# Optimization experiments

Measured on AMD Instinct MI355X. Metric: run time of the kernel, lower is better.

The kernel has to match this reference:

```python
import jax, jax.numpy as jnp
import numpy as np


def _ln(x, g, b, eps=1e-5):
    m = x.mean(-1, keepdims=True)
    v = ((x - m) ** 2).mean(-1, keepdims=True)
    return (x - m) / jnp.sqrt(v + eps) * g + b


def _conv(x, w, b, stride, pad, groups):
    # x: NCHW, w: OIHW (I = in_ch/groups)
    out = jax.lax.conv_general_dilated(
        x, w, (stride, stride), [(pad, pad), (pad, pad)],
        dimension_numbers=('NCHW', 'OIHW', 'NCHW'), feature_group_count=groups)
    return out + b[None, :, None, None]


def _gelu(x):
    return jax.nn.gelu(x, approximate=False)  # torch nn.GELU (exact erf)


def _forward(x, H, W, lpu_w, lpu_b, n1_g, n1_b, conv2d_w, conv2d_b, cn_g, cn_b,
             q_w, sr1_w, sr1_b, an1_g, an1_b, sr2_w, sr2_b, an2_g, an2_b,
             kv1_w, kv2_w, proj_w, proj_b, n2_g, n2_b,
             fc1_w, fc1_b, dw_w, dw_b, fc2_w, fc2_b):
    B, N, C = x.shape
    cd = C // 4          # conv_part_dim = 64
    ad = C - cd          # attn_part_dim = 192
    nh = 8
    hg = nh // 2         # heads per group
    hd = ad // nh        # head_dim = 24
    scale = hd ** -0.5
    # ---- LPU: depthwise 3x3 conv residual ----
    xi = x.transpose(0, 2, 1).reshape(B, C, H, W)
    xi = _conv(xi, lpu_w, lpu_b, 1, 1, C) + xi
    x = xi.reshape(B, C, N).transpose(0, 2, 1)
    # ---- Attention branch (pre-LN) ----
    y = _ln(x, n1_g, n1_b)
    cp, ap = y[..., :cd], y[..., cd:]
    # conv part: dense 3x3 conv (sr_ratio==8 -> kernel 3, pad 1), then LN+GELU in NLC
    cp = cp.reshape(B, H, W, cd).transpose(0, 3, 1, 2)
    cp = _conv(cp, conv2d_w, conv2d_b, 1, 1, 1).reshape(B, cd, N).transpose(0, 2, 1)
    cp = _gelu(_ln(cp, cn_g, cn_b))
    # attn part: dual spatial-reduction KV paths
    q = (ap @ q_w.T).reshape(B, N, nh, hd).transpose(0, 2, 1, 3)  # [B,nh,N,hd]
    x_ = ap.transpose(0, 2, 1).reshape(B, ad, H, W)
    x1 = _conv(x_, sr1_w, sr1_b, 8, 0, ad).reshape(B, ad, -1).transpose(0, 2, 1)  # [B,(H/8)(W/8),ad]
    x1 = _gelu(_ln(x1, an1_g, an1_b))
    x2 = _conv(x_, sr2_w, sr2_b, 4, 0, ad).reshape(B, ad, -1).transpose(0, 2, 1)  # [B,(H/4)(W/4),ad]
    x2 = _gelu(_ln(x2, an2_g, an2_b))
    kv1 = (x1 @ kv1_w.T).reshape(B, -1, 2, hg, hd).transpose(2, 0, 3, 1, 4)  # [2,B,hg,M1,hd]
    kv2 = (x2 @ kv2_w.T).reshape(B, -1, 2, hg, hd).transpose(2, 0, 3, 1, 4)

    def attn(qh, k, v):
        a = jax.nn.softmax(jnp.einsum('bhnd,bhmd->bhnm', qh, k) * scale, axis=-1)
        o = jnp.einsum('bhnm,bhmd->bhnd', a, v)
        return o.transpose(0, 2, 1, 3).reshape(B, N, -1)

    o1 = attn(q[:, :hg], kv1[0], kv1[1])
    o2 = attn(q[:, hg:], kv2[0], kv2[1])
    y = jnp.concatenate([o1, o2, cp], axis=-1) @ proj_w.T + proj_b
    x = x + y
    # ---- MLP with depthwise conv ----
    z = _ln(x, n2_g, n2_b) @ fc1_w.T + fc1_b
    hidc = z.shape[-1]
    z = z.transpose(0, 2, 1).reshape(B, hidc, H, W)
    z = _conv(z, dw_w, dw_b, 1, 1, hidc).reshape(B, hidc, N).transpose(0, 2, 1)
    z = _gelu(z) @ fc2_w.T + fc2_b
    return x + z


def setup_inputs() -> dict:
    key = jax.random.key(0)
    ks = jax.random.split(key, 16)
    B, H, W, C = 16, 56, 56, 256
    N = H * W
    cd, ad = C // 4, C * 3 // 4
    hid = 4 * C
    f = lambda i, shape, s=0.02: jax.random.normal(ks[i], shape, jnp.float32) * s
    return dict(
        x=jax.random.normal(ks[0], (B, N, C), jnp.float32),
        H=H, W=W,
        lpu_w=f(1, (C, 1, 3, 3), 0.1), lpu_b=jnp.zeros((C,), jnp.float32),
        n1_g=jnp.ones((C,), jnp.float32), n1_b=jnp.zeros((C,), jnp.float32),
        conv2d_w=f(2, (cd, cd, 3, 3), 0.05), conv2d_b=jnp.zeros((cd,), jnp.float32),
        cn_g=jnp.ones((cd,), jnp.float32), cn_b=jnp.zeros((cd,), jnp.float32),
        q_w=f(3, (ad, ad)),
        sr1_w=f(4, (ad, 1, 8, 8), 0.1), sr1_b=jnp.zeros((ad,), jnp.float32),
        an1_g=jnp.ones((ad,), jnp.float32), an1_b=jnp.zeros((ad,), jnp.float32),
        sr2_w=f(5, (ad, 1, 4, 4), 0.1), sr2_b=jnp.zeros((ad,), jnp.float32),
        an2_g=jnp.ones((ad,), jnp.float32), an2_b=jnp.zeros((ad,), jnp.float32),
        kv1_w=f(6, (ad, ad)), kv2_w=f(7, (ad, ad)),
        proj_w=f(8, (C, C)), proj_b=jnp.zeros((C,), jnp.float32),
        n2_g=jnp.ones((C,), jnp.float32), n2_b=jnp.zeros((C,), jnp.float32),
        fc1_w=f(9, (hid, C)), fc1_b=jnp.zeros((hid,), jnp.float32),
        dw_w=f(10, (hid, 1, 3, 3), 0.1), dw_b=jnp.zeros((hid,), jnp.float32),
        fc2_w=f(11, (C, hid)), fc2_b=jnp.zeros((C,), jnp.float32),
    )


def reference(x, H, W, lpu_w, lpu_b, n1_g, n1_b, conv2d_w, conv2d_b, cn_g, cn_b,
              q_w, sr1_w, sr1_b, an1_g, an1_b, sr2_w, sr2_b, an2_g, an2_b,
              kv1_w, kv2_w, proj_w, proj_b, n2_g, n2_b,
              fc1_w, fc1_b, dw_w, dw_b, fc2_w, fc2_b):
    return _forward(x, H, W, lpu_w, lpu_b, n1_g, n1_b, conv2d_w, conv2d_b, cn_g, cn_b,
                    q_w, sr1_w, sr1_b, an1_g, an1_b, sr2_w, sr2_b, an2_g, an2_b,
                    kv1_w, kv2_w, proj_w, proj_b, n2_g, n2_b,
                    fc1_w, fc1_b, dw_w, dw_b, fc2_w, fc2_b)
```

## Files before the change

### kernel.cpp

```cpp
#include <hip/hip_runtime.h>
#include <math.h>

#define BB   16
#define HH   56
#define WW   56
#define NN   (HH*WW)
#define CC   256
#define CD   64
#define AD   192
#define NH   8
#define HG   4
#define HD   24
#define HID  1024
#define M1   49
#define M2   196
#define BNR  (BB*NN)

typedef __attribute__((ext_vector_type(8))) short s8v;
typedef __attribute__((ext_vector_type(4))) short s4v;
typedef __attribute__((ext_vector_type(4))) float f4v;

__device__ __forceinline__ float gelu_f(float x) {
    float u = x * (1.0f + 0.044715f * x * x);
    float t = __expf(-1.5957691216f * u);
    return x * __builtin_amdgcn_rcpf(1.0f + t);
}
__device__ __forceinline__ ushort f2bf(float f) {
    union { float f; uint32_t u; } c; c.f = f;
    uint32_t u = c.u;
    return (ushort)((u + 0x7fffu + ((u >> 16) & 1u)) >> 16);
}
__device__ __forceinline__ float bf2f(ushort u) {
    union { uint32_t u; float f; } c; c.u = ((uint32_t)u) << 16;
    return c.f;
}
__device__ __forceinline__ void load_lds16(const void* gsrc, void* ldst) {
    __builtin_amdgcn_global_load_lds(
        (const __attribute__((address_space(1))) void*)gsrc,
        (__attribute__((address_space(3))) void*)ldst, 16, 0, 0);
}
__device__ __forceinline__ int xcd_swz(int bid, int nwg) {
    int q = nwg >> 3, r = nwg & 7;
    int x = bid & 7, i = bid >> 3;
    return (x < r ? x * (q + 1) : r * (q + 1) + (x - r) * q) + i;
}

__global__ __launch_bounds__(256) void wprep_kernel(
        const float* __restrict__ qw, const float* __restrict__ k1,
        const float* __restrict__ k2, const float* __restrict__ pw,
        const float* __restrict__ f1, const float* __restrict__ f2,
        const float* __restrict__ cw, const float* __restrict__ lw,
        const float* __restrict__ dw,
        ushort* __restrict__ wq, ushort* __restrict__ wkv1,
        ushort* __restrict__ wkv2, ushort* __restrict__ wpr,
        ushort* __restrict__ wf1, ushort* __restrict__ wf2,
        ushort* __restrict__ wcp, float* __restrict__ lpwt,
        float* __restrict__ dwwt) {
    int i = blockIdx.x * 256 + threadIdx.x;
    if (i < 36864) { wq[i] = f2bf(qw[i]); return; } i -= 36864;
    if (i < 36864) { wkv1[i] = f2bf(k1[i]); return; } i -= 36864;
    if (i < 36864) { wkv2[i] = f2bf(k2[i]); return; } i -= 36864;
    if (i < 65536) { wpr[i] = f2bf(pw[i]); return; } i -= 65536;
    if (i < 262144) { wf1[i] = f2bf(f1[i]); return; } i -= 262144;
    if (i < 262144) { wf2[i] = f2bf(f2[i]); return; } i -= 262144;
    if (i < 36864) {
        int co = i / 576, k = i - co * 576;
        int tap = k >> 6, ci = k & 63;
        wcp[i] = f2bf(cw[co * 576 + ci * 9 + tap]);
        return;
    } i -= 36864;
    if (i < 2304) { int c = i / 9, t = i - c * 9; lpwt[t * CC + c] = lw[i]; return; } i -= 2304;
    if (i < 9216) { int c = i / 9, t = i - c * 9; dwwt[t * HID + c] = dw[i]; }
}

__global__ __launch_bounds__(256) void lpu_kernel(const float* __restrict__ x,
        const float* __restrict__ wt, const float* __restrict__ bias,
        const float* __restrict__ n1g, const float* __restrict__ n1b,
        ushort* __restrict__ xbuf, ushort* __restrict__ ybuf) {
    int tid = threadIdx.x;
    int lane = tid & 63, wv = tid >> 6;
    int c = lane * 4;
    int grp = xcd_swz(blockIdx.x, NN / 16) * 4 + wv;
    int n0 = grp * 4;
    int h = n0 / WW, x0 = n0 - h * WW;
    int b = blockIdx.y;
    const float* xb = x + (size_t)b * NN * CC + c;
    float4 wreg[9];
#pragma unroll
    for (int t = 0; t < 9; ++t) wreg[t] = *(const float4*)(wt + t * CC + c);
    float4 bz = *(const float4*)(bias + c);
    float4 acc[4] = {bz, bz, bz, bz};
#pragma unroll
    for (int cx = 0; cx < 6; ++cx) {
        int wx = x0 + cx - 1;
        if ((unsigned)wx >= (unsigned)WW) continue;
#pragma unroll
        for (int ky = 0; ky < 3; ++ky) {
            int hy = h + ky - 1;
            if ((unsigned)hy >= (unsigned)HH) continue;
            float4 xv = *(const float4*)(xb + (size_t)(hy * WW + wx) * CC);
#pragma unroll
            for (int xo = 0; xo < 4; ++xo) {
                int kx = cx - xo;
                if (kx < 0 || kx > 2) continue;
                float4 wv4 = wreg[ky * 3 + kx];
                acc[xo].x = fmaf(xv.x, wv4.x, acc[xo].x);
                acc[xo].y = fmaf(xv.y, wv4.y, acc[xo].y);
                acc[xo].z = fmaf(xv.z, wv4.z, acc[xo].z);
                acc[xo].w = fmaf(xv.w, wv4.w, acc[xo].w);
            }
        }
    }
    float4 gv = *(const float4*)(n1g + c);
    float4 bv = *(const float4*)(n1b + c);
#pragma unroll
    for (int xo = 0; xo < 4; ++xo) {
        size_t o = ((size_t)b * NN + n0 + xo) * CC + c;
        float4 rv = *(const float4*)(x + o);
        float4 a = acc[xo];
        a.x += rv.x; a.y += rv.y; a.z += rv.z; a.w += rv.w;
        s4v xv4;
        xv4.x = (short)f2bf(a.x);
        xv4.y = (short)f2bf(a.y);
        xv4.z = (short)f2bf(a.z);
        xv4.w = (short)f2bf(a.w);
        *(s4v*)(xbuf + o) = xv4;
        float s = a.x + a.y + a.z + a.w;
        float sq = a.x * a.x + a.y * a.y + a.z * a.z + a.w * a.w;
#pragma unroll
        for (int off = 32; off >= 1; off >>= 1) {
            s += __shfl_xor(s, off, 64);
            sq += __shfl_xor(sq, off, 64);
        }
        float mean = s * (1.0f / 256.0f);
        float var = sq * (1.0f / 256.0f) - mean * mean;
        float rstd = rsqrtf(var + 1e-5f);
        s4v ov;
        ov.x = (short)f2bf((a.x - mean) * rstd * gv.x + bv.x);
        ov.y = (short)f2bf((a.y - mean) * rstd * gv.y + bv.y);
        ov.z = (short)f2bf((a.z - mean) * rstd * gv.z + bv.z);
        ov.w = (short)f2bf((a.w - mean) * rstd * gv.w + bv.w);
        *(s4v*)(ybuf + o) = ov;
    }
}

__global__ __launch_bounds__(256) void cpgemm_kernel(
        const ushort* __restrict__ y, const ushort* __restrict__ wt,
        const float* __restrict__ cb, const float* __restrict__ cng,
        const float* __restrict__ cnb, ushort* __restrict__ cat) {
    __shared__ __align__(16) ushort As[128 * 32];
    __shared__ __align__(16) ushort Ws[64 * 32];
    int tid = threadIdx.x;
    int wid = tid >> 6, lane = tid & 63;
    int rt = xcd_swz(blockIdx.x, BNR / 128) * 128;
    int r0 = tid >> 2, c0 = tid & 3;
    int r1 = r0 + 64;
    int tok0 = rt + r0, tok1 = rt + r1;
    int b0 = tok0 / NN, n0 = tok0 - b0 * NN, h0 = n0 / WW, w0 = n0 - h0 * WW;
    int b1 = tok1 / NN, n1 = tok1 - b1 * NN, h1 = n1 / WW, w1 = n1 - h1 * WW;
    const ushort* Wp = wt + (size_t)r0 * 576 + c0 * 8;
    int aw0 = (c0 ^ (r0 & 3)) << 3;
    f4v acc[2][4];
#pragma unroll
    for (int m = 0; m < 2; ++m)
#pragma unroll
        for (int n = 0; n < 4; ++n) acc[m][n] = (f4v)0.f;
    int lr = lane & 15, g4 = lane >> 4;
    int swz = (g4 ^ (lr & 3)) << 3;
    for (int kt = 0; kt < 576; kt += 32) {
        int tap = kt >> 6, ci0 = kt & 63;
        int t3 = tap / 3, dy = t3 - 1, dx = (tap - t3 * 3) - 1;
        s8v a0 = (s8v)0, a1 = (s8v)0;
        int hy0 = h0 + dy, wx0 = w0 + dx;
        if ((unsigned)hy0 < (unsigned)HH && (unsigned)wx0 < (unsigned)WW)
            a0 = *(const s8v*)(y + ((size_t)b0 * NN + hy0 * WW + wx0) * CC + ci0 + c0 * 8);
        int hy1 = h1 + dy, wx1 = w1 + dx;
        if ((unsigned)hy1 < (unsigned)HH && (unsigned)wx1 < (unsigned)WW)
            a1 = *(const s8v*)(y + ((size_t)b1 * NN + hy1 * WW + wx1) * CC + ci0 + c0 * 8);
        s8v wv = *(const s8v*)(Wp + kt);
        __syncthreads();
        *(s8v*)&As[r0 * 32 + aw0] = a0;
        *(s8v*)&As[r1 * 32 + aw0] = a1;
        *(s8v*)&Ws[r0 * 32 + aw0] = wv;
        __syncthreads();
        s8v af[2], bf[4];
#pragma unroll
        for (int m = 0; m < 2; ++m)
            af[m] = *(const s8v*)&As[(wid * 32 + m * 16 + lr) * 32 + swz];
#pragma unroll
        for (int n = 0; n < 4; ++n)
            bf[n] = *(const s8v*)&Ws[(n * 16 + lr) * 32 + swz];
#pragma unroll
        for (int m = 0; m < 2; ++m)
#pragma unroll
            for (int n = 0; n < 4; ++n)
                acc[m][n] = __builtin_amdgcn_mfma_f32_16x16x32_bf16(af[m], bf[n], acc[m][n], 0, 0, 0);
    }
    float gv[4], bv[4], cbv[4];
#pragma unroll
    for (int n = 0; n < 4; ++n) {
        int gc = n * 16 + lr;
        cbv[n] = cb[gc];
        gv[n] = cng[gc];
        bv[n] = cnb[gc];
    }
#pragma unroll
    for (int m = 0; m < 2; ++m)
#pragma unroll
        for (int r = 0; r < 4; ++r) {
            float s = 0.f, sq = 0.f;
#pragma unroll
            for (int n = 0; n < 4; ++n) {
                float v = acc[m][n][r] + cbv[n];
                acc[m][n][r] = v;
                s += v; sq += v * v;
            }
#pragma unroll
            for (int off = 1; off < 16; off <<= 1) {
                s += __shfl_xor(s, off, 64);
                sq += __shfl_xor(sq, off, 64);
            }
            float mean = s * (1.0f / 64.0f);
            float var = sq * (1.0f / 64.0f) - mean * mean;
            float rstd = rsqrtf(var + 1e-5f);
            int row = rt + wid * 32 + m * 16 + g4 * 4 + r;
            ushort* op = cat + (size_t)row * CC + 192;
#pragma unroll
            for (int n = 0; n < 4; ++n) {
                float v = (acc[m][n][r] - mean) * rstd * gv[n] + bv[n];
                op[n * 16 + lr] = f2bf(gelu_f(v));
            }
        }
}

template <int KS, int OW>
__global__ __launch_bounds__(192) void sr_kernel(const ushort* __restrict__ yap,
        const float* __restrict__ w, const float* __restrict__ bias,
        const float* __restrict__ g, const float* __restrict__ bt,
        ushort* __restrict__ out) {
    int ch = threadIdx.x;
    int m = blockIdx.x, b = blockIdx.y;
    int oh = m / OW, ow = m - oh * OW;
    const ushort* yb = yap + (size_t)b * NN * CC;
    float acc = bias[ch];
#pragma unroll
    for (int ky = 0; ky < KS; ++ky)
#pragma unroll
        for (int kx = 0; kx < KS; ++kx)
            acc = fmaf(bf2f(yb[(size_t)((oh * KS + ky) * WW + ow * KS + kx) * CC + ch]),
                       w[ch * KS * KS + ky * KS + kx], acc);
    __shared__ float red[2][3];
    float s = acc, sq = acc * acc;
#pragma unroll
    for (int off = 32; off >= 1; off >>= 1) {
        s += __shfl_xor(s, off, 64);
        sq += __shfl_xor(sq, off, 64);
    }
    int wv = threadIdx.x >> 6, lane = threadIdx.x & 63;
    if (lane == 0) { red[0][wv] = s; red[1][wv] = sq; }
    __syncthreads();
    s = red[0][0] + red[0][1] + red[0][2];
    sq = red[1][0] + red[1][1] + red[1][2];
    float mean = s * (1.0f / 192.0f);
    float var = sq * (1.0f / 192.0f) - mean * mean;
    float rstd = rsqrtf(var + 1e-5f);
    float v = (acc - mean) * rstd * g[ch] + bt[ch];
    out[((size_t)b * (OW * OW) + m) * AD + ch] = f2bf(gelu_f(v));
}

template <int MODE>
__global__ __launch_bounds__(512) void gemm_mfma(
        const ushort* __restrict__ A, int lda,
        const ushort* __restrict__ W, int K, int O,
        const float* __restrict__ bias,
        const ushort* __restrict__ res, int ldr,
        void* __restrict__ Cout, int ldc, int R) {
    __shared__ __align__(16) ushort As[2 * 256 * 32];
    __shared__ __align__(16) ushort Ws[2 * 128 * 32];
    int tid = threadIdx.x;
    int w8 = tid >> 6, lane = tid & 63;
    int wr = w8 >> 1, wc = w8 & 1;
    int nwg = gridDim.x * gridDim.y;
    int swzb = xcd_swz(blockIdx.y * gridDim.x + blockIdx.x, nwg);
    int rt = (swzb / gridDim.x) * 256, ot = (swzb % gridDim.x) * 128;
    int r0 = tid >> 2, cslot = tid & 3;
    int csrc = (cslot ^ (r0 & 3)) * 8;
    const ushort* Ap0 = A + (size_t)min(rt + r0, R - 1) * lda + csrc;
    const ushort* Ap1 = A + (size_t)min(rt + r0 + 128, R - 1) * lda + csrc;
    const ushort* Wp0 = W + (size_t)min(ot + r0, O - 1) * K + csrc;
    char* lA0 = (char*)As + w8 * 1024;
    char* lA1 = (char*)As + 8192 + w8 * 1024;
    char* lW0 = (char*)Ws + w8 * 1024;
    f4v acc[4][4];
#pragma unroll
    for (int m = 0; m < 4; ++m)
#pragma unroll
        for (int n = 0; n < 4; ++n) acc[m][n] = (f4v)0.f;
    int lr = lane & 15;
    int swz = ((lane >> 4) ^ (lr & 3)) << 3;
    load_lds16(Ap0, lA0);
    load_lds16(Ap1, lA1);
    load_lds16(Wp0, lW0);
    __syncthreads();
    int cur = 0;
    for (int kt = 0; kt < K; kt += 32) {
        if (kt + 32 < K) {
            int pa = (cur ^ 1) * 16384, pw = (cur ^ 1) * 8192;
            load_lds16(Ap0 + kt + 32, lA0 + pa);
            load_lds16(Ap1 + kt + 32, lA1 + pa);
            load_lds16(Wp0 + kt + 32, lW0 + pw);
        }
        const ushort* Ab = As + cur * 8192;
        const ushort* Wb = Ws + cur * 4096;
        s8v af[4], bf[4];
#pragma unroll
        for (int m = 0; m < 4; ++m)
            af[m] = *(const s8v*)&Ab[(wr * 64 + m * 16 + lr) * 32 + swz];
#pragma unroll
        for (int n = 0; n < 4; ++n)
            bf[n] = *(const s8v*)&Wb[(wc * 64 + n * 16 + lr) * 32 + swz];
#pragma unroll
        for (int m = 0; m < 4; ++m)
#pragma unroll
            for (int n = 0; n < 4; ++n)
                acc[m][n] = __builtin_amdgcn_mfma_f32_16x16x32_bf16(af[m], bf[n], acc[m][n], 0, 0, 0);
        __syncthreads();
        cur ^= 1;
    }
#pragma unroll
    for (int m = 0; m < 4; ++m)
#pragma unroll
        for (int n = 0; n < 4; ++n) {
            int gr = rt + wr * 64 + m * 16 + (lane >> 4) * 4;
            int gc = ot + wc * 64 + n * 16 + (lane & 15);
            if (gc >= O) continue;
#pragma unroll
            for (int r = 0; r < 4; ++r) {
                int row = gr + r;
                if (row >= R) continue;
                float v = acc[m][n][r];
                if (MODE & 1) v += bias[gc];
                if (MODE & 2) v += bf2f(res[(size_t)row * ldr + gc]);
                if (MODE & 4) ((ushort*)Cout)[(size_t)row * ldc + gc] = f2bf(v);
                else          ((float*)Cout)[(size_t)row * ldc + gc] = v;
            }
        }
}

__global__ __launch_bounds__(512) void projln_kernel(
        const ushort* __restrict__ A, const ushort* __restrict__ W,
        const float* __restrict__ bias,
        const float* __restrict__ n2g, const float* __restrict__ n2b,
        ushort* __restrict__ xbuf, ushort* __restrict__ ybuf) {
    __shared__ __align__(16) ushort As[128 * 32];
    __shared__ __align__(16) ushort Ws[256 * 32];
    int tid = threadIdx.x;
    int w8 = tid >> 6, lane = tid & 63;
    int rt = xcd_swz(blockIdx.x, BNR / 128) * 128;
    int r0 = tid >> 2, cslot = tid & 3;
    int csrc = (cslot ^ (r0 & 3)) * 8;
    const ushort* Ap0 = A + (size_t)(rt + r0) * CC + csrc;
    const ushort* Wp0 = W + (size_t)r0 * CC + csrc;
    const ushort* Wp1 = W + (size_t)(r0 + 128) * CC + csrc;
    char* lA0 = (char*)As + w8 * 1024;
    char* lW0 = (char*)Ws + w8 * 1024;
    char* lW1 = (char*)Ws + 8192 + w8 * 1024;
    int lr = lane & 15, g4 = lane >> 4;
    int swz = (g4 ^ (lr & 3)) << 3;
    f4v acc[16];
#pragma unroll
    for (int n = 0; n < 16; ++n) acc[n] = (f4v)(bias[n * 16 + lr]);
    for (int kt = 0; kt < CC; kt += 32) {
        __syncthreads();
        load_lds16(Ap0 + kt, lA0);
        load_lds16(Wp0 + kt, lW0);
        load_lds16(Wp1 + kt, lW1);
        __syncthreads();
        s8v af = *(const s8v*)&As[(w8 * 16 + lr) * 32 + swz];
#pragma unroll
        for (int n = 0; n < 16; ++n) {
            s8v bf = *(const s8v*)&Ws[(n * 16 + lr) * 32 + swz];
            acc[n] = __builtin_amdgcn_mfma_f32_16x16x32_bf16(af, bf, acc[n], 0, 0, 0);
        }
    }
#pragma unroll
    for (int r = 0; r < 4; ++r) {
        int row = rt + w8 * 16 + g4 * 4 + r;
        ushort* xr = xbuf + (size_t)row * CC;
        ushort* yr = ybuf + (size_t)row * CC;
        float s = 0.f, sq = 0.f;
#pragma unroll
        for (int n = 0; n < 16; ++n) {
            float v = acc[n][r] + bf2f(xr[n * 16 + lr]);
            acc[n][r] = v;
            s += v; sq += v * v;
        }
#pragma unroll
        for (int off = 1; off < 16; off <<= 1) {
            s += __shfl_xor(s, off, 64);
            sq += __shfl_xor(sq, off, 64);
        }
        float mean = s * (1.0f / 256.0f);
        float var = sq * (1.0f / 256.0f) - mean * mean;
        float rstd = rsqrtf(var + 1e-5f);
#pragma unroll
        for (int n = 0; n < 16; ++n) {
            int col = n * 16 + lr;
            float v = acc[n][r];
            xr[col] = f2bf(v);
            yr[col] = f2bf((v - mean) * rstd * n2g[col] + n2b[col]);
        }
    }
}

template <int M, int MP, int HOFF>
__global__ __launch_bounds__(256) void attn_mfma(const ushort* __restrict__ q,
        const ushort* __restrict__ kvb, ushort* __restrict__ cat) {
    constexpr int NT = MP / 16;
    constexpr int NCH = MP / 32;
    __shared__ __align__(16) ushort Kl[MP * 32];
    __shared__ __align__(16) ushort VT[32 * MP];
    int g = blockIdx.y, b = blockIdx.z;
    int h = HOFF + g;
    int tid = threadIdx.x;
    for (int i = tid; i < MP * 4; i += 256) ((s8v*)Kl)[i] = (s8v)0;
    for (int i = tid; i < MP * 4; i += 256) ((s8v*)VT)[i] = (s8v)0;
    __syncthreads();
    for (int u = tid; u < M * 3; u += 256) {
        int m = u / 3, d0 = u - m * 3;
        s8v kv8 = *(const s8v*)(kvb + ((size_t)b * M + m) * AD + g * HD + d0 * 8);
        *(s8v*)&Kl[m * 32 + ((d0 ^ (m & 3)) << 3)] = kv8;
    }
    for (int u = tid; u < M * 3; u += 256) {
        int m = u / 3, d0 = u - m * 3;
        s8v vv = *(const s8v*)(kvb + ((size_t)b * M + m) * AD + 96 + g * HD + d0 * 8);
        int c = m >> 5, mm = m & 31;
        int gg = (mm >> 2) & 3;
        int t = (mm & 3) + ((mm & 16) >> 2);
#pragma unroll
        for (int j = 0; j < 8; ++j) {
            int d = d0 * 8 + j;
            VT[d * MP + ((c * 4 + (gg ^ (d & 3))) << 3) + t] = (ushort)vv[j];
        }
    }
    __syncthreads();
    int w = tid >> 6, lane = tid & 63;
    int ln = lane & 15, g4 = lane >> 4;
    int swz = (g4 ^ (ln & 3)) << 3;
    const float scale = 0.20412414523193154f;
    for (int nt = 0; nt < 4; ++nt) {
        int nbase = blockIdx.x * 256 + nt * 64;
        if (nbase >= NN) break;
        int n0 = nbase + w * 16 + ln;
        s8v qf = (s8v)0;
        if (g4 < 3) qf = *(const s8v*)(q + ((size_t)b * NN + n0) * AD + h * HD + g4 * 8);
        f4v sa[NT];
#pragma unroll
        for (int t = 0; t < NT; ++t) sa[t] = (f4v)0.f;
#pragma unroll
        for (int t = 0; t < NT; ++t) {
            s8v kf = *(const s8v*)&Kl[(t * 16 + ln) * 32 + swz];
            sa[t] = __builtin_amdgcn_mfma_f32_16x16x32_bf16(kf, qf, sa[t], 0, 0, 0);
        }
        float mx = -3.0e38f;
#pragma unroll
        for (int t = 0; t < NT; ++t)
#pragma unroll
            for (int r = 0; r < 4; ++r) {
                int m = t * 16 + g4 * 4 + r;
                float v = (m < M) ? sa[t][r] * scale : -3.0e38f;
                sa[t][r] = v;
                mx = fmaxf(mx, v);
            }
        mx = fmaxf(mx, __shfl_xor(mx, 16, 64));
        mx = fmaxf(mx, __shfl_xor(mx, 32, 64));
        float sum = 0.f;
#pragma unroll
        for (int t = 0; t < NT; ++t)
#pragma unroll
            for (int r = 0; r < 4; ++r) {
                float p = __expf(sa[t][r] - mx);
                sa[t][r] = p;
                sum += p;
            }
        sum += __shfl_xor(sum, 16, 64);
        sum += __shfl_xor(sum, 32, 64);
        float inv = 1.0f / sum;
        f4v oa[2] = {(f4v)0.f, (f4v)0.f};
#pragma unroll
        for (int c = 0; c < NCH; ++c) {
            s8v pb;
#pragma unroll
            for (int t = 0; t < 4; ++t) {
                pb[t]     = (short)f2bf(sa[c * 2][t]);
                pb[4 + t] = (short)f2bf(sa[c * 2 + 1][t]);
            }
#pragma unroll
            for (int dt = 0; dt < 2; ++dt) {
                s8v vf = *(const s8v*)&VT[(dt * 16 + ln) * MP + c * 32 + swz];
                oa[dt] = __builtin_amdgcn_mfma_f32_16x16x32_bf16(vf, pb, oa[dt], 0, 0, 0);
            }
        }
        ushort* op = cat + ((size_t)b * NN + n0) * CC + h * HD;
        s4v o0;
#pragma unroll
        for (int r = 0; r < 4; ++r) o0[r] = (short)f2bf(oa[0][r] * inv);
        *(s4v*)(op + g4 * 4) = o0;
        if (g4 < 2) {
            s4v o1;
#pragma unroll
            for (int r = 0; r < 4; ++r) o1[r] = (short)f2bf(oa[1][r] * inv);
            *(s4v*)(op + 16 + g4 * 4) = o1;
        }
    }
}

__global__ __launch_bounds__(256) void dwconv_kernel(const ushort* __restrict__ z1,
        const float* __restrict__ wt, const float* __restrict__ bias,
        ushort* __restrict__ z2) {
    int bid = xcd_swz(blockIdx.x, HH * 7);
    int h = bid / 7, bx = bid - h * 7;
    int b = blockIdx.y;
    int c = (threadIdx.x & 127) * 8;
    int x0 = bx * 8 + (threadIdx.x >> 7) * 4;
    const ushort* zrow = z1 + ((size_t)b * NN + h * WW) * HID + c;
    float wreg[9][8];
#pragma unroll
    for (int t = 0; t < 9; ++t) {
        float4 w0 = *(const float4*)(wt + t * HID + c);
        float4 w1 = *(const float4*)(wt + t * HID + c + 4);
        wreg[t][0] = w0.x; wreg[t][1] = w0.y; wreg[t][2] = w0.z; wreg[t][3] = w0.w;
        wreg[t][4] = w1.x; wreg[t][5] = w1.y; wreg[t][6] = w1.z; wreg[t][7] = w1.w;
    }
    float acc[4][8];
    {
        float4 b0 = *(const float4*)(bias + c);
        float4 b1 = *(const float4*)(bias + c + 4);
#pragma unroll
        for (int xo = 0; xo < 4; ++xo) {
            acc[xo][0] = b0.x; acc[xo][1] = b0.y; acc[xo][2] = b0.z; acc[xo][3] = b0.w;
            acc[xo][4] = b1.x; acc[xo][5] = b1.y; acc[xo][6] = b1.z; acc[xo][7] = b1.w;
        }
    }
#pragma unroll
    for (int cx = 0; cx < 6; ++cx) {
        int wx = x0 + cx - 1;
        if ((unsigned)wx >= (unsigned)WW) continue;
#pragma unroll
        for (int ky = 0; ky < 3; ++ky) {
            int hy = h + ky - 1;
            if ((unsigned)hy >= (unsigned)HH) continue;
            s8v v = *(const s8v*)(zrow + ((size_t)(ky - 1) * WW + wx) * HID);
            float vf[8];
#pragma unroll
            for (int j = 0; j < 8; ++j) vf[j] = bf2f((ushort)v[j]);
#pragma unroll
            for (int xo = 0; xo < 4; ++xo) {
                int kx = cx - xo;
                if (kx < 0 || kx > 2) continue;
#pragma unroll
                for (int j = 0; j < 8; ++j)
                    acc[xo][j] = fmaf(vf[j], wreg[ky * 3 + kx][j], acc[xo][j]);
            }
        }
    }
    ushort* zo = z2 + ((size_t)b * NN + h * WW + x0) * HID + c;
#pragma unroll
    for (int xo = 0; xo < 4; ++xo) {
        s8v o;
#pragma unroll
        for (int j = 0; j < 8; ++j) o[j] = (short)f2bf(gelu_f(acc[xo][j]));
        *(s8v*)(zo + (size_t)xo * HID) = o;
    }
}

extern "C" void kernel_launch(void* const* d_in, const int* in_sizes, int n_in,
                              void* d_out, int out_size, void* d_ws, size_t ws_size,
                              hipStream_t stream) {
    const float* x      = (const float*)d_in[0];
    const float* lpu_w  = (const float*)d_in[3];
    const float* lpu_b  = (const float*)d_in[4];
    const float* n1_g   = (const float*)d_in[5];
    const float* n1_b   = (const float*)d_in[6];
    const float* c2_w   = (const float*)d_in[7];
    const float* c2_b   = (const float*)d_in[8];
    const float* cn_g   = (const float*)d_in[9];
    const float* cn_b   = (const float*)d_in[10];
    const float* q_w    = (const float*)d_in[11];
    const float* sr1_w  = (const float*)d_in[12];
    const float* sr1_b  = (const float*)d_in[13];
    const float* an1_g  = (const float*)d_in[14];
    const float* an1_b  = (const float*)d_in[15];
    const float* sr2_w  = (const float*)d_in[16];
    const float* sr2_b  = (const float*)d_in[17];
    const float* an2_g  = (const float*)d_in[18];
    const float* an2_b  = (const float*)d_in[19];
    const float* kv1_w  = (const float*)d_in[20];
    const float* kv2_w  = (const float*)d_in[21];
    const float* proj_w = (const float*)d_in[22];
    const float* proj_b = (const float*)d_in[23];
    const float* n2_g   = (const float*)d_in[24];
    const float* n2_b   = (const float*)d_in[25];
    const float* fc1_w  = (const float*)d_in[26];
    const float* fc1_b  = (const float*)d_in[27];
    const float* dw_w   = (const float*)d_in[28];
    const float* dw_b   = (const float*)d_in[29];
    const float* fc2_w  = (const float*)d_in[30];
    const float* fc2_b  = (const float*)d_in[31];
    float* out = (float*)d_out;

    char* ws = (char*)d_ws;
    size_t off = 0;
    auto allocB = [&](size_t bytes) {
        char* p = ws + off;
        off += ((bytes + 255) & ~(size_t)255);
        return p;
    };
    ushort* xbuf = (ushort*)allocB((size_t)BNR * CC * 2);
    ushort* ybuf = (ushort*)allocB((size_t)BNR * CC * 2);
    ushort* wq   = (ushort*)allocB((size_t)AD * AD * 2);
    ushort* wkv1 = (ushort*)allocB((size_t)AD * AD * 2);
    ushort* wkv2 = (ushort*)allocB((size_t)AD * AD * 2);
    ushort* wpr  = (ushort*)allocB((size_t)CC * CC * 2);
    ushort* wf1  = (ushort*)allocB((size_t)HID * CC * 2);
    ushort* wf2  = (ushort*)allocB((size_t)CC * HID * 2);
    ushort* wcp  = (ushort*)allocB((size_t)64 * 576 * 2);
    float*  lpwt = (float*)allocB((size_t)9 * CC * 4);
    float*  dwwt = (float*)allocB((size_t)9 * HID * 4);
    size_t zmark = off;
    ushort* cat  = (ushort*)allocB((size_t)BNR * CC * 2);
    ushort* qbuf = (ushort*)allocB((size_t)BNR * AD * 2);
    ushort* x1g  = (ushort*)allocB((size_t)BB * M1 * AD * 2);
    ushort* x2g  = (ushort*)allocB((size_t)BB * M2 * AD * 2);
    ushort* kv1b = (ushort*)allocB((size_t)BB * M1 * AD * 2);
    ushort* kv2b = (ushort*)allocB((size_t)BB * M2 * AD * 2);

    int CB2 = 1;
    for (int cb = 16; cb >= 1; cb >>= 1) {
        if (zmark + 2 * (size_t)cb * NN * HID * 2 <= ws_size) { CB2 = cb; break; }
    }

    dim3 b256(256), b512(512);
    wprep_kernel<<<dim3(2925), b256, 0, stream>>>(
        q_w, kv1_w, kv2_w, proj_w, fc1_w, fc2_w, c2_w, lpu_w, dw_w,
        wq, wkv1, wkv2, wpr, wf1, wf2, wcp, lpwt, dwwt);
    lpu_kernel<<<dim3(NN / 16, BB), b256, 0, stream>>>(x, lpwt, lpu_b, n1_g, n1_b, xbuf, ybuf);
    cpgemm_kernel<<<dim3(BNR / 128), b256, 0, stream>>>(ybuf, wcp, c2_b, cn_g, cn_b, cat);
    gemm_mfma<4><<<dim3(2, BNR / 256), b512, 0, stream>>>(
        ybuf + CD, CC, wq, AD, AD, nullptr, nullptr, 0, qbuf, AD, BNR);
    sr_kernel<8, 7><<<dim3(M1, BB), dim3(192), 0, stream>>>(ybuf + CD, sr1_w, sr1_b, an1_g, an1_b, x1g);
    sr_kernel<4, 14><<<dim3(M2, BB), dim3(192), 0, stream>>>(ybuf + CD, sr2_w, sr2_b, an2_g, an2_b, x2g);
    gemm_mfma<4><<<dim3(2, (BB * M1 + 255) / 256), b512, 0, stream>>>(
        x1g, AD, wkv1, AD, AD, nullptr, nullptr, 0, kv1b, AD, BB * M1);
    gemm_mfma<4><<<dim3(2, (BB * M2 + 255) / 256), b512, 0, stream>>>(
        x2g, AD, wkv2, AD, AD, nullptr, nullptr, 0, kv2b, AD, BB * M2);
    attn_mfma<M1, 64, 0><<<dim3((NN + 255) / 256, HG, BB), b256, 0, stream>>>(qbuf, kv1b, cat);
    attn_mfma<M2, 224, HG><<<dim3((NN + 255) / 256, HG, BB), b256, 0, stream>>>(qbuf, kv2b, cat);
    projln_kernel<<<dim3(BNR / 128), b512, 0, stream>>>(
        cat, wpr, proj_b, n2_g, n2_b, xbuf, ybuf);
    ushort* z1 = (ushort*)(ws + zmark);
    ushort* z2 = z1 + (size_t)CB2 * NN * HID;
    for (int c0 = 0; c0 < BB; c0 += CB2) {
        size_t tokoff = (size_t)c0 * NN;
        int Rr = CB2 * NN;
        gemm_mfma<5><<<dim3(HID / 128, (Rr + 255) / 256), b512, 0, stream>>>(
            ybuf + tokoff * CC, CC, wf1, CC, HID, fc1_b, nullptr, 0, z1, HID, Rr);
        dwconv_kernel<<<dim3(HH * 7, CB2), b256, 0, stream>>>(z1, dwwt, dw_b, z2);
        gemm_mfma<3><<<dim3(CC / 128, (Rr + 255) / 256), b512, 0, stream>>>(
            z2, HID, wf2, HID, CC, fc2_b, xbuf + tokoff * CC, CC, out + tokoff * CC, CC, Rr);
    }
}
```

Measured before the change: 388.2 us.

## Run MLP depthwise conv in packed fp16 and feed fp16 into fc2 MFMA

The fc1 GEMM now writes fp16 instead of bf16. The depthwise 3x3 conv then loads fp16 weights and accumulates in packed half2 FMAs, with no per-element bf16-to-float conversions. Its GELU output is stored as fp16, and fc2 runs on fp16 MFMA using fp16 weights. This is meant to halve the VALU work in the dwconv and remove conversion overhead. The cost is reduced accumulation precision over the 9 taps and a risk of fp16 overflow.

```diff
diff --git a/kernel.cpp b/kernel.cpp
--- a/kernel.cpp
+++ b/kernel.cpp
@@ -19,6 +19,8 @@
 typedef __attribute__((ext_vector_type(8))) short s8v;
 typedef __attribute__((ext_vector_type(4))) short s4v;
 typedef __attribute__((ext_vector_type(4))) float f4v;
+typedef __attribute__((ext_vector_type(8))) _Float16 h8v;
+typedef __attribute__((ext_vector_type(2))) _Float16 h2v;
 
 __device__ __forceinline__ float gelu_f(float x) {
     float u = x * (1.0f + 0.044715f * x * x);
@@ -33,6 +35,10 @@
 __device__ __forceinline__ float bf2f(ushort u) {
     union { uint32_t u; float f; } c; c.u = ((uint32_t)u) << 16;
     return c.f;
+}
+__device__ __forceinline__ ushort f2h(float f) {
+    union { _Float16 h; ushort u; } c; c.h = (_Float16)f;
+    return c.u;
 }
 __device__ __forceinline__ void load_lds16(const void* gsrc, void* ldst) {
     __builtin_amdgcn_global_load_lds(
@@ -55,14 +61,14 @@
         ushort* __restrict__ wkv2, ushort* __restrict__ wpr,
         ushort* __restrict__ wf1, ushort* __restrict__ wf2,
         ushort* __restrict__ wcp, float* __restrict__ lpwt,
-        float* __restrict__ dwwt) {
+        ushort* __restrict__ dwwth) {
     int i = blockIdx.x * 256 + threadIdx.x;
     if (i < 36864) { wq[i] = f2bf(qw[i]); return; } i -= 36864;
     if (i < 36864) { wkv1[i] = f2bf(k1[i]); return; } i -= 36864;
     if (i < 36864) { wkv2[i] = f2bf(k2[i]); return; } i -= 36864;
     if (i < 65536) { wpr[i] = f2bf(pw[i]); return; } i -= 65536;
     if (i < 262144) { wf1[i] = f2bf(f1[i]); return; } i -= 262144;
-    if (i < 262144) { wf2[i] = f2bf(f2[i]); return; } i -= 262144;
+    if (i < 262144) { wf2[i] = f2h(f2[i]); return; } i -= 262144;
     if (i < 36864) {
         int co = i / 576, k = i - co * 576;
         int tap = k >> 6, ci = k & 63;
@@ -70,7 +76,7 @@
         return;
     } i -= 36864;
     if (i < 2304) { int c = i / 9, t = i - c * 9; lpwt[t * CC + c] = lw[i]; return; } i -= 2304;
-    if (i < 9216) { int c = i / 9, t = i - c * 9; dwwt[t * HID + c] = dw[i]; }
+    if (i < 9216) { int c = i / 9, t = i - c * 9; dwwth[t * HID + c] = f2h(dw[i]); }
 }
 
 __global__ __launch_bounds__(256) void lpu_kernel(const float* __restrict__ x,
@@ -268,7 +274,7 @@
     out[((size_t)b * (OW * OW) + m) * AD + ch] = f2bf(gelu_f(v));
 }
 
-template <int MODE>
+template <int MODE, int F16 = 0>
 __global__ __launch_bounds__(512) void gemm_mfma(
         const ushort* __restrict__ A, int lda,
         const ushort* __restrict__ W, int K, int O,
@@ -322,8 +328,15 @@
 #pragma unroll
         for (int m = 0; m < 4; ++m)
 #pragma unroll
-            for (int n = 0; n < 4; ++n)
-                acc[m][n] = __builtin_amdgcn_mfma_f32_16x16x32_bf16(af[m], bf[n], acc[m][n], 0, 0, 0);
+            for (int n = 0; n < 4; ++n) {
+                if (F16) {
+                    h8v ah = *(const h8v*)&af[m];
+                    h8v bh = *(const h8v*)&bf[n];
+                    acc[m][n] = __builtin_amdgcn_mfma_f32_16x16x32_f16(ah, bh, acc[m][n], 0, 0, 0);
+                } else {
+                    acc[m][n] = __builtin_amdgcn_mfma_f32_16x16x32_bf16(af[m], bf[n], acc[m][n], 0, 0, 0);
+                }
+            }
         __syncthreads();
         cur ^= 1;
     }
@@ -341,8 +354,9 @@
                 float v = acc[m][n][r];
                 if (MODE & 1) v += bias[gc];
                 if (MODE & 2) v += bf2f(res[(size_t)row * ldr + gc]);
-                if (MODE & 4) ((ushort*)Cout)[(size_t)row * ldc + gc] = f2bf(v);
-                else          ((float*)Cout)[(size_t)row * ldc + gc] = v;
+                if (MODE & 4)      ((ushort*)Cout)[(size_t)row * ldc + gc] = f2bf(v);
+                else if (MODE & 8) ((ushort*)Cout)[(size_t)row * ldc + gc] = f2h(v);
+                else               ((float*)Cout)[(size_t)row * ldc + gc] = v;
             }
         }
 }
@@ -516,7 +530,7 @@
 }
 
 __global__ __launch_bounds__(256) void dwconv_kernel(const ushort* __restrict__ z1,
-        const float* __restrict__ wt, const float* __restrict__ bias,
+        const ushort* __restrict__ wt, const float* __restrict__ bias,
         ushort* __restrict__ z2) {
     int bid = xcd_swz(blockIdx.x, HH * 7);
     int h = bid / 7, bx = bid - h * 7;
@@ -524,23 +538,27 @@
     int c = (threadIdx.x & 127) * 8;
     int x0 = bx * 8 + (threadIdx.x >> 7) * 4;
     const ushort* zrow = z1 + ((size_t)b * NN + h * WW) * HID + c;
-    float wreg[9][8];
+    h2v wreg[9][4];
 #pragma unroll
     for (int t = 0; t < 9; ++t) {
-        float4 w0 = *(const float4*)(wt + t * HID + c);
-        float4 w1 = *(const float4*)(wt + t * HID + c + 4);
-        wreg[t][0] = w0.x; wreg[t][1] = w0.y; wreg[t][2] = w0.z; wreg[t][3] = w0.w;
-        wreg[t][4] = w1.x; wreg[t][5] = w1.y; wreg[t][6] = w1.z; wreg[t][7] = w1.w;
-    }
-    float acc[4][8];
+        s8v w8 = *(const s8v*)(wt + t * HID + c);
+        const h2v* wp = (const h2v*)&w8;
+#pragma unroll
+        for (int p = 0; p < 4; ++p) wreg[t][p] = wp[p];
+    }
+    h2v acc[4][4];
     {
         float4 b0 = *(const float4*)(bias + c);
         float4 b1 = *(const float4*)(bias + c + 4);
-#pragma unroll
-        for (int xo = 0; xo < 4; ++xo) {
-            acc[xo][0] = b0.x; acc[xo][1] = b0.y; acc[xo][2] = b0.z; acc[xo][3] = b0.w;
-            acc[xo][4] = b1.x; acc[xo][5] = b1.y; acc[xo][6] = b1.z; acc[xo][7] = b1.w;
-        }
+        h2v bz[4];
+        bz[0][0] = (_Float16)b0.x; bz[0][1] = (_Float16)b0.y;
+        bz[1][0] = (_Float16)b0.z; bz[1][1] = (_Float16)b0.w;
+        bz[2][0] = (_Float16)b1.x; bz[2][1] = (_Float16)b1.y;
+        bz[3][0] = (_Float16)b1.z; bz[3][1] = (_Float16)b1.w;
+#pragma unroll
+        for (int xo = 0; xo < 4; ++xo)
+#pragma unroll
+            for (int p = 0; p < 4; ++p) acc[xo][p] = bz[p];
     }
 #pragma unroll
     for (int cx = 0; cx < 6; ++cx) {
@@ -551,16 +569,14 @@
             int hy = h + ky - 1;
             if ((unsigned)hy >= (unsigned)HH) continue;
             s8v v = *(const s8v*)(zrow + ((size_t)(ky - 1) * WW + wx) * HID);
-            float vf[8];
-#pragma unroll
-            for (int j = 0; j < 8; ++j) vf[j] = bf2f((ushort)v[j]);
+            const h2v* v2 = (const h2v*)&v;
 #pragma unroll
             for (int xo = 0; xo < 4; ++xo) {
                 int kx = cx - xo;
                 if (kx < 0 || kx > 2) continue;
 #pragma unroll
-                for (int j = 0; j < 8; ++j)
-                    acc[xo][j] = fmaf(vf[j], wreg[ky * 3 + kx][j], acc[xo][j]);
+                for (int p = 0; p < 4; ++p)
+                    acc[xo][p] = v2[p] * wreg[ky * 3 + kx][p] + acc[xo][p];
             }
         }
     }
@@ -569,7 +585,10 @@
     for (int xo = 0; xo < 4; ++xo) {
         s8v o;
 #pragma unroll
-        for (int j = 0; j < 8; ++j) o[j] = (short)f2bf(gelu_f(acc[xo][j]));
+        for (int p = 0; p < 4; ++p) {
+            o[p * 2]     = (short)f2h(gelu_f((float)acc[xo][p][0]));
+            o[p * 2 + 1] = (short)f2h(gelu_f((float)acc[xo][p][1]));
+        }
         *(s8v*)(zo + (size_t)xo * HID) = o;
     }
 }
@@ -626,7 +645,7 @@
     ushort* wf2  = (ushort*)allocB((size_t)CC * HID * 2);
     ushort* wcp  = (ushort*)allocB((size_t)64 * 576 * 2);
     float*  lpwt = (float*)allocB((size_t)9 * CC * 4);
-    float*  dwwt = (float*)allocB((size_t)9 * HID * 4);
+    ushort* dwwt = (ushort*)allocB((size_t)9 * HID * 2);
     size_t zmark = off;
     ushort* cat  = (ushort*)allocB((size_t)BNR * CC * 2);
     ushort* qbuf = (ushort*)allocB((size_t)BNR * AD * 2);
@@ -663,10 +682,10 @@
     for (int c0 = 0; c0 < BB; c0 += CB2) {
         size_t tokoff = (size_t)c0 * NN;
         int Rr = CB2 * NN;
-        gemm_mfma<5><<<dim3(HID / 128, (Rr + 255) / 256), b512, 0, stream>>>(
+        gemm_mfma<9><<<dim3(HID / 128, (Rr + 255) / 256), b512, 0, stream>>>(
             ybuf + tokoff * CC, CC, wf1, CC, HID, fc1_b, nullptr, 0, z1, HID, Rr);
         dwconv_kernel<<<dim3(HH * 7, CB2), b256, 0, stream>>>(z1, dwwt, dw_b, z2);
-        gemm_mfma<3><<<dim3(CC / 128, (Rr + 255) / 256), b512, 0, stream>>>(
+        gemm_mfma<3, 1><<<dim3(CC / 128, (Rr + 255) / 256), b512, 0, stream>>>(
             z2, HID, wf2, HID, CC, fc2_b, xbuf + tokoff * CC, CC, out + tokoff * CC, CC, Rr);
     }
 }
```

After: 374.2 us. 3.6% less time.
